# Optimization experiments

Measured on AMD Instinct MI355X. Metric: run time of the kernel, lower is better.

Reference implementation:

```python
import jax, jax.numpy as jnp
import numpy as np

B, N, D = 16, 2048, 64

def setup_inputs() -> dict:
    key = jax.random.key(0)
    kq, kk, kv = jax.random.split(key, 3)
    queries = jax.random.normal(kq, (B, N, D), dtype=jnp.float32)
    keys = jax.random.normal(kk, (B, N, D), dtype=jnp.float32)
    values = jax.random.normal(kv, (B, N, D), dtype=jnp.float32)
    scaling_factor = jnp.asarray(np.sqrt(D), dtype=jnp.float32)
    return {"queries": queries, "keys": keys, "values": values, "scaling_factor": scaling_factor}

def reference(queries, keys, values, scaling_factor):
    # scores: [B, N, N] = Q K^T / scale
    scores = jnp.einsum('bqd,bkd->bqk', queries, keys) / scaling_factor
    atn = jax.nn.softmax(scores, axis=2)
    return jnp.einsum('bqk,bkd->bqd', atn, values)
```

## Files before the change

kernel.cpp:

```cpp
#include <hip/hip_runtime.h>
#include <hip/hip_bf16.h>

#define BATCH 16
#define SEQ 2048
#define DIM 64

typedef __attribute__((ext_vector_type(8))) __bf16 bf16x8;
typedef __attribute__((ext_vector_type(8))) unsigned short u16x8;
typedef __attribute__((ext_vector_type(4))) unsigned int u32x4;
typedef __attribute__((ext_vector_type(16))) float f32x16;

#if __has_builtin(__builtin_amdgcn_exp2f)
#define EXP2F(x) __builtin_amdgcn_exp2f(x)
#else
#define EXP2F(x) __expf(0.69314718055994531f * (x))
#endif

__device__ __forceinline__ unsigned short f2bf_hw(float f) {
    __bf16 h = (__bf16)f;
    return __builtin_bit_cast(unsigned short, h);
}

__device__ __forceinline__ unsigned int pk_bf16(float lo, float hi) {
    unsigned int a = f2bf_hw(lo), b = f2bf_hw(hi);
    return a | (b << 16);
}

__device__ __forceinline__ bf16x8 ld_bf8(const unsigned short* p) {
    u16x8 u = *(const u16x8*)p;
    return __builtin_bit_cast(bf16x8, u);
}

__device__ __forceinline__ void async_copy16(const unsigned short* g, unsigned short* l) {
    __builtin_amdgcn_global_load_lds(
        (const __attribute__((address_space(1))) unsigned int*)g,
        (__attribute__((address_space(3))) unsigned int*)l, 16, 0, 0);
}

__global__ __launch_bounds__(256)
void preconvert_kv(const float* __restrict__ K, const float* __restrict__ V,
                   unsigned short* __restrict__ Ks, unsigned short* __restrict__ Vts) {
    __shared__ float vt[128 * 65];
    const int tid = threadIdx.x;
    const int b = blockIdx.x >> 4;
    const int t = blockIdx.x & 15;
    const int kt = t * 128;

    {
        const float* src = V + ((size_t)(b * SEQ + kt)) * DIM;
        #pragma unroll
        for (int p = 0; p < 8; ++p) {
            const int f = p * 256 + tid;
            const int row = f >> 4, c4 = (f & 15) << 2;
            float4 x = *(const float4*)(src + row * DIM + c4);
            vt[row * 65 + c4 + 0] = x.x; vt[row * 65 + c4 + 1] = x.y;
            vt[row * 65 + c4 + 2] = x.z; vt[row * 65 + c4 + 3] = x.w;
        }
    }
    {
        const float* src = K + ((size_t)(b * SEQ + kt)) * DIM;
        unsigned short* dst = Ks + ((size_t)(b * 16 + t)) * 8192;
        #pragma unroll
        for (int p = 0; p < 4; ++p) {
            const int cid = p * 256 + tid;
            const int key = cid >> 3, g = cid & 7;
            const int d0 = (g >> 1) * 16 + (g & 1) * 8;
            float4 x0 = *(const float4*)(src + key * DIM + d0);
            float4 x1 = *(const float4*)(src + key * DIM + d0 + 4);
            u16x8 o;
            o[0] = f2bf_hw(x0.x); o[1] = f2bf_hw(x0.y); o[2] = f2bf_hw(x0.z); o[3] = f2bf_hw(x0.w);
            o[4] = f2bf_hw(x1.x); o[5] = f2bf_hw(x1.y); o[6] = f2bf_hw(x1.z); o[7] = f2bf_hw(x1.w);
            *(u16x8*)(dst + (g * 128 + key) * 8) = o;
        }
    }
    __syncthreads();
    {
        unsigned short* dst = Vts + ((size_t)(b * 16 + t)) * 8192;
        #pragma unroll
        for (int p = 0; p < 4; ++p) {
            const int cid = p * 256 + tid;
            const int g = cid >> 6, d = cid & 63;
            const int k0 = (g >> 1) * 16 + (g & 1) * 8;
            u16x8 o;
            #pragma unroll
            for (int j = 0; j < 8; ++j) o[j] = f2bf_hw(vt[(k0 + j) * 65 + d]);
            *(u16x8*)(dst + (g * 64 + d) * 8) = o;
        }
    }
}

__global__ __launch_bounds__(256, 2)
void attn_flash_kernel(const float* __restrict__ Q,
                       const unsigned short* __restrict__ Ks,
                       const unsigned short* __restrict__ Vts,
                       const float* __restrict__ scaling,
                       float* __restrict__ O) {
    extern __shared__ char smem[];
    unsigned short* lds = (unsigned short*)smem;

    const int tid  = threadIdx.x;
    const int w    = tid >> 6;
    const int lane = tid & 63;
    const int m    = lane & 31;
    const int h    = lane >> 5;
    const int qw   = w & 1;
    const int kw   = w >> 1;

    const int b  = blockIdx.x >> 5;
    const int q0 = (blockIdx.x & 31) * 64;

    const float csc = 1.4426950408889634f / scaling[0];

    bf16x8 aq[4];
    {
        const float* qsrc = Q + ((size_t)(b * SEQ + q0 + qw * 32 + m)) * DIM + h * 8;
        #pragma unroll
        for (int c = 0; c < 4; ++c) {
            float4 x0 = *(const float4*)(qsrc + c * 16);
            float4 x1 = *(const float4*)(qsrc + c * 16 + 4);
            u32x4 pk;
            pk[0] = pk_bf16(x0.x * csc, x0.y * csc);
            pk[1] = pk_bf16(x0.z * csc, x0.w * csc);
            pk[2] = pk_bf16(x1.x * csc, x1.y * csc);
            pk[3] = pk_bf16(x1.z * csc, x1.w * csc);
            aq[c] = __builtin_bit_cast(bf16x8, pk);
        }
    }

    f32x16 Oacc[2];
    #pragma unroll
    for (int dt = 0; dt < 2; ++dt)
        #pragma unroll
        for (int r = 0; r < 16; ++r) Oacc[dt][r] = 0.f;
    float psum = 0.f;

    unsigned short* Kt = lds + kw * 16384;
    unsigned short* Vt = lds + kw * 16384 + 8192;
    const unsigned short* gsrc = ((w & 1) ? Vts : Ks) + ((size_t)(b * 16 + kw * 8)) * 8192;
    unsigned short* ldst = lds + w * 8192;

    for (int it = 0; it < 8; ++it) {
        __syncthreads();
        const unsigned short* gt = gsrc + (size_t)it * 8192;
        #pragma unroll
        for (int j = 0; j < 16; ++j)
            async_copy16(gt + j * 512 + lane * 8, ldst + j * 512);
        __syncthreads();

        #pragma unroll
        for (int t = 0; t < 4; ++t) {
            f32x16 S;
            #pragma unroll
            for (int r = 0; r < 16; ++r) S[r] = 0.f;
            #pragma unroll
            for (int c = 0; c < 4; ++c) {
                bf16x8 bk = ld_bf8(&Kt[((c * 2 + h) * 128 + t * 32 + m) * 8]);
                S = __builtin_amdgcn_mfma_f32_32x32x16_bf16(bk, aq[c], S, 0, 0, 0);
            }
            unsigned int d0[8], ds[8];
            float ps = 0.f;
            #pragma unroll
            for (int k = 0; k < 4; ++k) {
                float p0 = EXP2F(S[4 * k + 0]);
                float p1 = EXP2F(S[4 * k + 1]);
                float p2 = EXP2F(S[4 * k + 2]);
                float p3 = EXP2F(S[4 * k + 3]);
                ps += (p0 + p1) + (p2 + p3);
                d0[2 * k + 0] = pk_bf16(p0, p1);
                d0[2 * k + 1] = pk_bf16(p2, p3);
            }
            psum += ps;
            #pragma unroll
            for (int i = 0; i < 8; ++i) ds[i] = (unsigned int)__shfl_xor((int)d0[i], 32);
            #pragma unroll
            for (int c2 = 0; c2 < 2; ++c2) {
                u32x4 bw;
                bw[0] = h ? ds[4 * c2 + 2] : d0[4 * c2 + 0];
                bw[1] = h ? ds[4 * c2 + 3] : d0[4 * c2 + 1];
                bw[2] = h ? d0[4 * c2 + 2] : ds[4 * c2 + 0];
                bw[3] = h ? d0[4 * c2 + 3] : ds[4 * c2 + 1];
                bf16x8 pb = __builtin_bit_cast(bf16x8, bw);
                const int kc = 2 * t + c2;
                #pragma unroll
                for (int dt = 0; dt < 2; ++dt) {
                    bf16x8 bv = ld_bf8(&Vt[((kc * 2 + h) * 64 + dt * 32 + m) * 8]);
                    Oacc[dt] = __builtin_amdgcn_mfma_f32_32x32x16_bf16(bv, pb, Oacc[dt], 0, 0, 0);
                }
            }
        }
    }

    float lhalf = psum + __shfl_xor(psum, 32);
    __syncthreads();
    float* fl = (float*)smem;
    if (kw == 1) {
        float* dst = fl + (w - 2) * 2112 + lane * 33;
        #pragma unroll
        for (int dt = 0; dt < 2; ++dt)
            #pragma unroll
            for (int r = 0; r < 16; ++r) dst[dt * 16 + r] = Oacc[dt][r];
        dst[32] = lhalf;
    }
    __syncthreads();
    if (kw == 0) {
        const float* pr = fl + w * 2112 + lane * 33;
        const float invl = 1.0f / (lhalf + pr[32]);
        float* orow = O + ((size_t)(b * SEQ + q0 + qw * 32 + m)) * DIM;
        #pragma unroll
        for (int dt = 0; dt < 2; ++dt) {
            #pragma unroll
            for (int k = 0; k < 4; ++k) {
                float4 o4;
                o4.x = (Oacc[dt][4 * k + 0] + pr[dt * 16 + 4 * k + 0]) * invl;
                o4.y = (Oacc[dt][4 * k + 1] + pr[dt * 16 + 4 * k + 1]) * invl;
                o4.z = (Oacc[dt][4 * k + 2] + pr[dt * 16 + 4 * k + 2]) * invl;
                o4.w = (Oacc[dt][4 * k + 3] + pr[dt * 16 + 4 * k + 3]) * invl;
                *(float4*)(orow + dt * 32 + 8 * k + 4 * h) = o4;
            }
        }
    }
}

extern "C" void kernel_launch(void* const* d_in, const int* in_sizes, int n_in,
                              void* d_out, int out_size, void* d_ws, size_t ws_size,
                              hipStream_t stream) {
    const float* Q = (const float*)d_in[0];
    const float* K = (const float*)d_in[1];
    const float* V = (const float*)d_in[2];
    const float* scaling = (const float*)d_in[3];
    float* O = (float*)d_out;

    unsigned short* Ks  = (unsigned short*)d_ws;
    unsigned short* Vts = Ks + (size_t)BATCH * 16 * 8192;

    preconvert_kv<<<dim3(BATCH * 16), dim3(256), 0, stream>>>(K, V, Ks, Vts);
    attn_flash_kernel<<<dim3(BATCH * (SEQ / 64)), dim3(256), 65536, stream>>>(Q, Ks, Vts, scaling, O);
}
```

Measured before the change: 108.2 us.

## Read K/V fragments directly from global memory with 4-way key split per block

Drops the LDS staging of K and V tiles and has each wave load its MFMA operands straight from global memory (relying on L2/cache reuse). Each block now handles 32 queries, with four waves each covering a quarter of the keys, and the partial outputs are combined through a small shared buffer. The grid doubles, the batch index is swizzled across blocks, and occupancy is raised to 4 blocks per CU. This removes the per-iteration barriers and the 64KB LDS footprint. In exchange, every wave issues more global loads with no sharing between waves, so the kernel depends much more on cache hit rates.

New measurement: 126.2 us. +16.6%, slower.

```diff
diff --git a/kernel.cpp b/kernel.cpp
--- a/kernel.cpp
+++ b/kernel.cpp
@@ -26,15 +26,9 @@
     return a | (b << 16);
 }
 
-__device__ __forceinline__ bf16x8 ld_bf8(const unsigned short* p) {
+__device__ __forceinline__ bf16x8 ld_bf8_g(const unsigned short* p) {
     u16x8 u = *(const u16x8*)p;
     return __builtin_bit_cast(bf16x8, u);
-}
-
-__device__ __forceinline__ void async_copy16(const unsigned short* g, unsigned short* l) {
-    __builtin_amdgcn_global_load_lds(
-        (const __attribute__((address_space(1))) unsigned int*)g,
-        (__attribute__((address_space(3))) unsigned int*)l, 16, 0, 0);
 }
 
 __global__ __launch_bounds__(256)
@@ -89,31 +83,29 @@
     }
 }
 
-__global__ __launch_bounds__(256, 2)
+__global__ __launch_bounds__(256, 4)
 void attn_flash_kernel(const float* __restrict__ Q,
                        const unsigned short* __restrict__ Ks,
                        const unsigned short* __restrict__ Vts,
                        const float* __restrict__ scaling,
                        float* __restrict__ O) {
-    extern __shared__ char smem[];
-    unsigned short* lds = (unsigned short*)smem;
+    __shared__ float comb[3 * 64 * 33];
 
     const int tid  = threadIdx.x;
     const int w    = tid >> 6;
     const int lane = tid & 63;
     const int m    = lane & 31;
     const int h    = lane >> 5;
-    const int qw   = w & 1;
-    const int kw   = w >> 1;
-
-    const int b  = blockIdx.x >> 5;
-    const int q0 = (blockIdx.x & 31) * 64;
+
+    const int x  = blockIdx.x;
+    const int b  = ((x & 7) << 1) | ((x >> 3) & 1);
+    const int q0 = (x >> 4) * 32;
 
     const float csc = 1.4426950408889634f / scaling[0];
 
     bf16x8 aq[4];
     {
-        const float* qsrc = Q + ((size_t)(b * SEQ + q0 + qw * 32 + m)) * DIM + h * 8;
+        const float* qsrc = Q + ((size_t)(b * SEQ + q0 + m)) * DIM + h * 8;
         #pragma unroll
         for (int c = 0; c < 4; ++c) {
             float4 x0 = *(const float4*)(qsrc + c * 16);
@@ -134,19 +126,12 @@
         for (int r = 0; r < 16; ++r) Oacc[dt][r] = 0.f;
     float psum = 0.f;
 
-    unsigned short* Kt = lds + kw * 16384;
-    unsigned short* Vt = lds + kw * 16384 + 8192;
-    const unsigned short* gsrc = ((w & 1) ? Vts : Ks) + ((size_t)(b * 16 + kw * 8)) * 8192;
-    unsigned short* ldst = lds + w * 8192;
-
-    for (int it = 0; it < 8; ++it) {
-        __syncthreads();
-        const unsigned short* gt = gsrc + (size_t)it * 8192;
-        #pragma unroll
-        for (int j = 0; j < 16; ++j)
-            async_copy16(gt + j * 512 + lane * 8, ldst + j * 512);
-        __syncthreads();
-
+    const unsigned short* Kbase = Ks + ((size_t)(b * 16 + w * 4)) * 8192;
+    const unsigned short* Vbase = Vts + ((size_t)(b * 16 + w * 4)) * 8192;
+
+    for (int it = 0; it < 4; ++it) {
+        const unsigned short* Kt = Kbase + (size_t)it * 8192;
+        const unsigned short* Vt = Vbase + (size_t)it * 8192;
         #pragma unroll
         for (int t = 0; t < 4; ++t) {
             f32x16 S;
@@ -154,7 +139,7 @@
             for (int r = 0; r < 16; ++r) S[r] = 0.f;
             #pragma unroll
             for (int c = 0; c < 4; ++c) {
-                bf16x8 bk = ld_bf8(&Kt[((c * 2 + h) * 128 + t * 32 + m) * 8]);
+                bf16x8 bk = ld_bf8_g(&Kt[((c * 2 + h) * 128 + t * 32 + m) * 8]);
                 S = __builtin_amdgcn_mfma_f32_32x32x16_bf16(bk, aq[c], S, 0, 0, 0);
             }
             unsigned int d0[8], ds[8];
@@ -183,38 +168,40 @@
                 const int kc = 2 * t + c2;
                 #pragma unroll
                 for (int dt = 0; dt < 2; ++dt) {
-                    bf16x8 bv = ld_bf8(&Vt[((kc * 2 + h) * 64 + dt * 32 + m) * 8]);
+                    bf16x8 bv = ld_bf8_g(&Vt[((kc * 2 + h) * 64 + dt * 32 + m) * 8]);
                     Oacc[dt] = __builtin_amdgcn_mfma_f32_32x32x16_bf16(bv, pb, Oacc[dt], 0, 0, 0);
                 }
             }
         }
     }
 
-    float lhalf = psum + __shfl_xor(psum, 32);
+    float lq = psum + __shfl_xor(psum, 32);
+    if (w > 0) {
+        float* dst = comb + ((w - 1) * 64 + lane) * 33;
+        #pragma unroll
+        for (int dt = 0; dt < 2; ++dt)
+            #pragma unroll
+            for (int r = 0; r < 16; ++r) dst[dt * 16 + r] = Oacc[dt][r];
+        dst[32] = lq;
+    }
     __syncthreads();
-    float* fl = (float*)smem;
-    if (kw == 1) {
-        float* dst = fl + (w - 2) * 2112 + lane * 33;
-        #pragma unroll
-        for (int dt = 0; dt < 2; ++dt)
-            #pragma unroll
-            for (int r = 0; r < 16; ++r) dst[dt * 16 + r] = Oacc[dt][r];
-        dst[32] = lhalf;
-    }
-    __syncthreads();
-    if (kw == 0) {
-        const float* pr = fl + w * 2112 + lane * 33;
-        const float invl = 1.0f / (lhalf + pr[32]);
-        float* orow = O + ((size_t)(b * SEQ + q0 + qw * 32 + m)) * DIM;
+    if (w == 0) {
+        const float* p0 = comb + (0 * 64 + lane) * 33;
+        const float* p1 = comb + (1 * 64 + lane) * 33;
+        const float* p2 = comb + (2 * 64 + lane) * 33;
+        const float invl = 1.0f / (lq + p0[32] + p1[32] + p2[32]);
+        float* orow = O + ((size_t)(b * SEQ + q0 + m)) * DIM;
         #pragma unroll
         for (int dt = 0; dt < 2; ++dt) {
             #pragma unroll
             for (int k = 0; k < 4; ++k) {
                 float4 o4;
-                o4.x = (Oacc[dt][4 * k + 0] + pr[dt * 16 + 4 * k + 0]) * invl;
-                o4.y = (Oacc[dt][4 * k + 1] + pr[dt * 16 + 4 * k + 1]) * invl;
-                o4.z = (Oacc[dt][4 * k + 2] + pr[dt * 16 + 4 * k + 2]) * invl;
-                o4.w = (Oacc[dt][4 * k + 3] + pr[dt * 16 + 4 * k + 3]) * invl;
+                #pragma unroll
+                for (int j = 0; j < 4; ++j) {
+                    const int r = 4 * k + j;
+                    ((float*)&o4)[j] = (Oacc[dt][r] + p0[dt * 16 + r] + p1[dt * 16 + r]
+                                        + p2[dt * 16 + r]) * invl;
+                }
                 *(float4*)(orow + dt * 32 + 8 * k + 4 * h) = o4;
             }
         }
@@ -234,5 +221,5 @@
     unsigned short* Vts = Ks + (size_t)BATCH * 16 * 8192;
 
     preconvert_kv<<<dim3(BATCH * 16), dim3(256), 0, stream>>>(K, V, Ks, Vts);
-    attn_flash_kernel<<<dim3(BATCH * (SEQ / 64)), dim3(256), 65536, stream>>>(Q, Ks, Vts, scaling, O);
-}
+    attn_flash_kernel<<<dim3(BATCH * (SEQ / 32)), dim3(256), 0, stream>>>(Q, Ks, Vts, scaling, O);
+}
```
